# Performance work log

Hardware: AMD Instinct MI355X
Metric: run time of the kernel (lower is better)

The kernel has to match this reference:

```python
import jax, jax.numpy as jnp
import numpy as np

B, N, D, N_HOPS = 32, 1024, 128, 3
EPS = 1e-6


def setup_inputs() -> dict:
    key = jax.random.key(0)
    k1, k2, k3, k4 = jax.random.split(key, 4)
    # binary base adjacency (non-trainable buffer in the torch module)
    adj = (jax.random.uniform(k1, (N, N)) < 0.05).astype(jnp.float32)
    adj_weight = jax.random.uniform(k2, (B, N, N), dtype=jnp.float32)
    x = jax.random.normal(k3, (B, N, D), dtype=jnp.float32)
    W = jax.random.normal(k4, (D, D), dtype=jnp.float32) * 0.05
    b = jnp.zeros((D,), jnp.float32)
    a2 = jnp.ones((D,), jnp.float32)   # LayerNorm scale
    b2 = jnp.zeros((D,), jnp.float32)  # LayerNorm shift
    return {"x": x, "adj_weight": adj_weight, "adj": adj, "W": W, "b": b, "a2": a2, "b2": b2}


def _conv(x, adj_weight, adj):
    # adj_power squares the matrix each hop: hop h uses A^(2^h).
    # mask_h = (A^(2^h) == 1.0); weighted hop = (W^(2^h)) * mask_h.
    # propagate(edge_index from dense_to_sparse) == sum_j Wmask[b,j,i] * x[b,j]  (A^T x)
    A = adj            # [N, N]
    Wp = adj_weight    # [B, N, N]
    agg = jnp.zeros_like(x)
    for h in range(N_HOPS):
        mask = (A == 1.0).astype(x.dtype)          # [N, N]
        Wh = Wp * mask                              # [B, N, N]
        agg = agg + jnp.einsum('bji,bjd->bid', Wh, x)
        if h < N_HOPS - 1:
            A = A @ A
            Wp = jnp.matmul(Wp, Wp)
    return agg


def reference(x, adj_weight, adj, W, b, a2, b2):
    agg = _conv(x, adj_weight, adj)
    h = jnp.einsum('bnd,od->bno', agg, W) + b + x   # Linear + residual
    mean = jnp.mean(h, axis=-1, keepdims=True)
    std = jnp.std(h, axis=-1, keepdims=True, ddof=1)  # torch.std is unbiased
    y = a2 * (h - mean) / (std + EPS) + b2
    return y  # dropout p=0 (eval) -> identity
```

## Files before the change

kernel.cpp:

```cpp
#include <hip/hip_runtime.h>

#define NN 1024
#define BB 32
#define DD 128
#define EPSF 1e-6f
#define CAP 16384

typedef __bf16 bf16x8 __attribute__((ext_vector_type(8)));
typedef float  f32x4  __attribute__((ext_vector_type(4)));
typedef unsigned short u16x8 __attribute__((ext_vector_type(8)));

__device__ __forceinline__ float bf2f(unsigned short u) {
  union { unsigned int i; float f; } v; v.i = ((unsigned int)u) << 16; return v.f;
}
__device__ __forceinline__ unsigned short f2bf(float f) {
  union { float f; unsigned int i; } v; v.f = f;
  unsigned int r = v.i + 0x7fffu + ((v.i >> 16) & 1u);
  return (unsigned short)(r >> 16);
}


__global__ __launch_bounds__(256) void convert_wp(const float* __restrict__ src,
    unsigned short* __restrict__ Wp, unsigned short* __restrict__ WpT) {
  __shared__ float tile[64][65];
  const int b = blockIdx.z;
  const int c0 = blockIdx.x * 64, r0 = blockIdx.y * 64;
  const int t = threadIdx.x;
  const int rr = t >> 3, cb = (t & 7) * 8;
  const size_t base = (size_t)b * NN * NN;
#pragma unroll
  for (int p = 0; p < 2; ++p) {
    const int r = rr + p * 32;
    const float* srow = src + base + (size_t)(r0 + r) * NN + c0 + cb;
    f32x4 v0 = *(const f32x4*)srow;
    f32x4 v1 = *(const f32x4*)(srow + 4);
    u16x8 w;
#pragma unroll
    for (int j = 0; j < 4; ++j) { w[j] = f2bf(v0[j]); w[4 + j] = f2bf(v1[j]); }
    *(u16x8*)(Wp + base + (size_t)(r0 + r) * NN + c0 + cb) = w;
#pragma unroll
    for (int j = 0; j < 4; ++j) { tile[r][cb + j] = v0[j]; tile[r][cb + 4 + j] = v1[j]; }
  }
  __syncthreads();
#pragma unroll
  for (int p = 0; p < 2; ++p) {
    const int r = rr + p * 32;
    u16x8 w;
#pragma unroll
    for (int j = 0; j < 8; ++j) w[j] = f2bf(tile[cb + j][r]);
    *(u16x8*)(WpT + base + (size_t)(c0 + r) * NN + r0 + cb) = w;
  }
}

__global__ __launch_bounds__(256) void convert_x(const float* __restrict__ x,
    unsigned short* __restrict__ xT) {
  __shared__ float tile[32][33];
  const int b = blockIdx.z;
  const int d0 = blockIdx.x * 32, n0 = blockIdx.y * 32;
  const int tx = threadIdx.x, ty = threadIdx.y;
#pragma unroll
  for (int s = 0; s < 4; ++s) {
    int rr = ty + s * 8;
    tile[rr][tx] = x[(size_t)b * NN * DD + (size_t)(n0 + rr) * DD + d0 + tx];
  }
  __syncthreads();
#pragma unroll
  for (int s = 0; s < 4; ++s) {
    int rr = ty + s * 8;
    xT[(size_t)b * DD * NN + (size_t)(d0 + rr) * NN + n0 + tx] = f2bf(tile[tx][rr]);
  }
}

__global__ __launch_bounds__(256) void mask0cvt(const float* __restrict__ adj,
    unsigned char* __restrict__ mcode, unsigned short* __restrict__ adjbf,
    unsigned short* __restrict__ adjTbf) {
  __shared__ float tile[32][33];
  const int i0 = blockIdx.x * 32, j0 = blockIdx.y * 32;
  const int tx = threadIdx.x, ty = threadIdx.y;
#pragma unroll
  for (int s = 0; s < 4; ++s) {
    int rr = ty + s * 8;
    float v = adj[(size_t)(j0 + rr) * NN + i0 + tx];
    adjbf[(size_t)(j0 + rr) * NN + i0 + tx] = f2bf(v);
    tile[rr][tx] = v;
  }
  __syncthreads();
#pragma unroll
  for (int s = 0; s < 4; ++s) {
    int rr = ty + s * 8;
    float v = tile[tx][rr];
    adjTbf[(size_t)(i0 + rr) * NN + j0 + tx] = f2bf(v);
    mcode[(size_t)(i0 + rr) * NN + j0 + tx] = (v == 1.0f) ? 1 : 0;
  }
}

#define BM 128
#define BN 128
#define BK 32
#define NIT (NN / BK)

__device__ __forceinline__ void async_cp16(const void* g, void* l) {
  __builtin_amdgcn_global_load_lds((const __attribute__((address_space(1))) void*)g,
                                   (__attribute__((address_space(3))) void*)l, 16, 0, 0);
}

struct EpiWcomb {
  const unsigned short* WpT;
  const unsigned char* mcode;
  unsigned short* out;
  __device__ __forceinline__ void operator()(int b, int i, int j, float v) const {
    size_t bnn = (size_t)b * (size_t)NN * NN;
    size_t idx = (size_t)i * NN + j;
    unsigned char mc = mcode[idx];
    float r = (mc & 2) ? v : 0.f;
    if (mc & 1) r += bf2f(WpT[bnn + idx]);
    out[bnn + idx] = f2bf(r);
  }
};

struct EpiAgg {
  float* agg;
  __device__ __forceinline__ void operator()(int b, int i, int d, float v) const {
    agg[(size_t)b * NN * DD + (size_t)i * DD + d] = v;
  }
};

struct EpiSq1 {
  unsigned short* A2;
  unsigned short* A2T;
  unsigned char* mcode;
  __device__ __forceinline__ void operator()(int b, int m, int n, float v) const {
    unsigned short bv = f2bf(v);
    A2[(size_t)m * NN + n] = bv;
    A2T[(size_t)n * NN + m] = bv;
    if (v == 1.0f) mcode[(size_t)n * NN + m] |= 2;
  }
};

struct EpiSq2 {
  unsigned int* entries;
  int* nnz;
  __device__ __forceinline__ void operator()(int b, int m, int n, float v) const {
    if (v == 1.0f) {
      int idx = atomicAdd(nnz, 1);
      if (idx < CAP) entries[idx] = ((unsigned)m << 16) | (unsigned)n;
    }
  }
};

template <typename Epi>
__global__ __launch_bounds__(256) void gemm_bt(const unsigned short* __restrict__ Abase,
    const unsigned short* __restrict__ Bbase, size_t sA, size_t sB, int swz, Epi epi) {
  __shared__ __align__(16) unsigned short As[3 * BM * BK];
  __shared__ __align__(16) unsigned short Bs[3 * BN * BK];
  const int b = blockIdx.z;
  int bx = blockIdx.x, by = blockIdx.y;
  if (swz) {
    int lin = bx + (by << 3);
    int r = lin & 7, s = lin >> 3;
    bx = ((r & 3) << 1) | (s & 1);
    by = ((r >> 2) << 2) | (s >> 1);
  }
  const int tm = bx * BM;
  const int tn = by * BN;
  const unsigned short* A = Abase + (size_t)b * sA;
  const unsigned short* B = Bbase + (size_t)b * sB;
  const int tid = threadIdx.x;
  const int w = tid >> 6, l = tid & 63;
  const int lr = l >> 2, lc = l & 3;
  const int fr = l & 15, quad = l >> 4;
  const int moff = (w & 1) * 64, noff = (w >> 1) * 64;
  f32x4 acc[4][4];
#pragma unroll
  for (int mi = 0; mi < 4; ++mi)
#pragma unroll
    for (int ni = 0; ni < 4; ++ni) acc[mi][ni] = (f32x4){0.f, 0.f, 0.f, 0.f};

  auto issue = [&](int kt, int buf) {
    unsigned short* Ad = As + buf * (BM * BK);
    unsigned short* Bd = Bs + buf * (BN * BK);
#pragma unroll
    for (int s = 0; s < 2; ++s) {
      const int rb = (w + s * 4) * 16;
      int r = rb + lr;
      int kc = lc ^ ((r >> 1) & 3);
      async_cp16(A + (size_t)(tm + r) * NN + kt * BK + kc * 8, (void*)(Ad + rb * BK));
      async_cp16(B + (size_t)(tn + r) * NN + kt * BK + kc * 8, (void*)(Bd + rb * BK));
    }
  };
  auto compute = [&](int buf) {
    const unsigned short* Ab = As + buf * (BM * BK);
    const unsigned short* Bb = Bs + buf * (BN * BK);
    bf16x8 af[4], bfr[4];
#pragma unroll
    for (int mi = 0; mi < 4; ++mi) {
      int r = moff + mi * 16 + fr;
      int kc = quad ^ ((r >> 1) & 3);
      af[mi] = *(const bf16x8*)(Ab + r * BK + kc * 8);
    }
#pragma unroll
    for (int ni = 0; ni < 4; ++ni) {
      int r = noff + ni * 16 + fr;
      int kc = quad ^ ((r >> 1) & 3);
      bfr[ni] = *(const bf16x8*)(Bb + r * BK + kc * 8);
    }
#pragma unroll
    for (int mi = 0; mi < 4; ++mi)
#pragma unroll
      for (int ni = 0; ni < 4; ++ni)
        acc[mi][ni] = __builtin_amdgcn_mfma_f32_16x16x32_bf16(af[mi], bfr[ni], acc[mi][ni], 0, 0, 0);
  };

  issue(0, 0); issue(1, 1); issue(2, 2);
#pragma unroll 1
  for (int kt = 0; kt < NIT - 3; ++kt) {
    asm volatile("s_waitcnt vmcnt(8)" ::: "memory");
    __builtin_amdgcn_s_barrier();
    asm volatile("" ::: "memory");
    compute(kt % 3);
    asm volatile("" ::: "memory");
    __builtin_amdgcn_s_barrier();
    asm volatile("" ::: "memory");
    issue(kt + 3, kt % 3);
  }
  asm volatile("s_waitcnt vmcnt(8)" ::: "memory");
  __builtin_amdgcn_s_barrier();
  asm volatile("" ::: "memory");
  compute((NIT - 3) % 3);
  asm volatile("s_waitcnt vmcnt(4)" ::: "memory");
  __builtin_amdgcn_s_barrier();
  asm volatile("" ::: "memory");
  compute((NIT - 2) % 3);
  asm volatile("s_waitcnt vmcnt(0)" ::: "memory");
  __builtin_amdgcn_s_barrier();
  asm volatile("" ::: "memory");
  compute((NIT - 1) % 3);
  asm volatile("" ::: "memory");

#pragma unroll
  for (int mi = 0; mi < 4; ++mi)
#pragma unroll
    for (int ni = 0; ni < 4; ++ni)
#pragma unroll
      for (int t = 0; t < 4; ++t)
        epi(b, tm + moff + mi * 16 + quad * 4 + t, tn + noff + ni * 16 + fr, acc[mi][ni][t]);
}

__global__ __launch_bounds__(256) void hop2_fix(const unsigned short* __restrict__ Wp,
    const unsigned short* __restrict__ WpT, const int* __restrict__ nnz,
    const unsigned int* __restrict__ entries, unsigned short* __restrict__ WcombT) {
  int n = *nnz;
  if (n > CAP) n = CAP;
  if (n == 0) return;
  __shared__ float rbuf[256];
  const int b = blockIdx.x;
  const size_t bnn = (size_t)b * NN * NN;
  for (int e = blockIdx.y; e < n; e += gridDim.y) {
    unsigned int ent = entries[e];
    int j = ent >> 16, i = ent & 0xFFFF;
    float s = 0.f;
    for (int k = threadIdx.x; k < NN; k += 256) {
      float u = 0.f, v = 0.f;
      const unsigned short* wj  = Wp  + bnn + (size_t)j * NN;
      const unsigned short* wtk = WpT + bnn + (size_t)k * NN;
      const unsigned short* wk  = Wp  + bnn + (size_t)k * NN;
      const unsigned short* wti = WpT + bnn + (size_t)i * NN;
      for (int t = 0; t < NN; ++t) {
        u += bf2f(wj[t]) * bf2f(wtk[t]);
        v += bf2f(wk[t]) * bf2f(wti[t]);
      }
      s += u * v;
    }
    rbuf[threadIdx.x] = s;
    __syncthreads();
    for (int off = 128; off > 0; off >>= 1) {
      if (threadIdx.x < off) rbuf[threadIdx.x] += rbuf[threadIdx.x + off];
      __syncthreads();
    }
    if (threadIdx.x == 0) {
      size_t idx = bnn + (size_t)i * NN + j;
      WcombT[idx] = f2bf(bf2f(WcombT[idx]) + rbuf[0]);
    }
    __syncthreads();
  }
}

#define ROWS_PER_BLK 32
__global__ __launch_bounds__(256) void fused_out(const float* agg, const float* __restrict__ x,
    const float* __restrict__ W, const float* __restrict__ bias,
    const float* __restrict__ g2, const float* __restrict__ bsh, float* out) {
  __shared__ unsigned short Wl[128 * 136];
  __shared__ float ar[256];
  __shared__ float xr[256];
  __shared__ float wred[8];
  const int tid = threadIdx.x;
  for (int e = tid; e < 16384; e += 256) Wl[(e >> 7) * 136 + (e & 127)] = f2bf(W[e]);
  const int half = tid >> 7, o = tid & 127;
  const int w = tid >> 6, lane = tid & 63;
  const float bo = bias[o], go = g2[o], b2o = bsh[o];
  const size_t row0 = (size_t)blockIdx.x * ROWS_PER_BLK;
  for (int rr = 0; rr < ROWS_PER_BLK; rr += 2) {
    const size_t rbase = (row0 + rr) * DD;
    __syncthreads();
    ar[tid] = agg[rbase + tid];
    xr[tid] = x[rbase + tid];
    __syncthreads();
    float hv = bo + xr[half * 128 + o];
    const unsigned short* wrow = &Wl[o * 136];
    const float* arow = &ar[half * 128];
#pragma unroll
    for (int d8 = 0; d8 < 16; ++d8) {
      bf16x8 wv = *(const bf16x8*)(wrow + d8 * 8);
#pragma unroll
      for (int t = 0; t < 8; ++t) hv += (float)wv[t] * arow[d8 * 8 + t];
    }
    float s = hv, q = hv * hv;
#pragma unroll
    for (int off = 32; off > 0; off >>= 1) {
      s += __shfl_xor(s, off);
      q += __shfl_xor(q, off);
    }
    if (lane == 0) { wred[w] = s; wred[4 + w] = q; }
    __syncthreads();
    float st = wred[half * 2] + wred[half * 2 + 1];
    float qt = wred[4 + half * 2] + wred[4 + half * 2 + 1];
    float mean = st * (1.0f / 128.0f);
    float var = (qt - 128.0f * mean * mean) * (1.0f / 127.0f);
    var = fmaxf(var, 0.0f);
    float stdv = sqrtf(var);
    out[rbase + tid] = go * (hv - mean) / (stdv + EPSF) + b2o;
  }
}

extern "C" void kernel_launch(void* const* d_in, const int* in_sizes, int n_in,
                              void* d_out, int out_size, void* d_ws, size_t ws_size,
                              hipStream_t stream) {
  (void)in_sizes; (void)n_in; (void)out_size; (void)ws_size;
  const float* x    = (const float*)d_in[0];
  const float* adjw = (const float*)d_in[1];
  const float* adj  = (const float*)d_in[2];
  const float* W    = (const float*)d_in[3];
  const float* bias = (const float*)d_in[4];
  const float* a2   = (const float*)d_in[5];
  const float* b2   = (const float*)d_in[6];
  float* out = (float*)d_out;

  char* ws = (char*)d_ws;
  unsigned short* Wp_bf   = (unsigned short*)(ws);
  unsigned short* WpT_bf  = (unsigned short*)(ws + 67108864);
  unsigned short* WcombT  = (unsigned short*)(ws + 134217728);
  unsigned short* xT_bf   = (unsigned short*)(ws + 201326592);
  unsigned short* adj_bf  = (unsigned short*)(ws + 209715200);
  unsigned short* adjT_bf = (unsigned short*)(ws + 211812352);
  unsigned short* A2_bf   = (unsigned short*)(ws + 213909504);
  unsigned short* A2T_bf  = (unsigned short*)(ws + 216006656);
  unsigned char* mcode    = (unsigned char*)(ws + 218103808);
  unsigned int* entries   = (unsigned int*)(ws + 219152384);
  int* nnz2               = (int*)(ws + 219217920);
  float* agg = out;

  hipMemsetAsync(nnz2, 0, 4, stream);

  dim3 blk32(32, 8, 1);
  convert_wp<<<dim3(16, 16, 32), 256, 0, stream>>>(adjw, Wp_bf, WpT_bf);
  convert_x<<<dim3(4, 32, 32), blk32, 0, stream>>>(x, xT_bf);
  mask0cvt<<<dim3(32, 32, 1), blk32, 0, stream>>>(adj, mcode, adj_bf, adjT_bf);

  EpiSq1 es1{A2_bf, A2T_bf, mcode};
  gemm_bt<EpiSq1><<<dim3(8, 8, 1), 256, 0, stream>>>(adj_bf, adjT_bf, 0, 0, 1, es1);
  EpiSq2 es2{entries, nnz2};
  gemm_bt<EpiSq2><<<dim3(8, 8, 1), 256, 0, stream>>>(A2_bf, A2T_bf, 0, 0, 1, es2);

  EpiWcomb e1{WpT_bf, mcode, WcombT};
  gemm_bt<EpiWcomb><<<dim3(8, 8, 32), 256, 0, stream>>>(WpT_bf, Wp_bf,
      (size_t)NN * NN, (size_t)NN * NN, 1, e1);

  hop2_fix<<<dim3(32, 8, 1), 256, 0, stream>>>(Wp_bf, WpT_bf, nnz2, entries, WcombT);

  EpiAgg e2{agg};
  gemm_bt<EpiAgg><<<dim3(8, 1, 32), 256, 0, stream>>>(WcombT, xT_bf,
      (size_t)NN * NN, (size_t)DD * NN, 0, e2);

  fused_out<<<dim3(1024, 1, 1), 256, 0, stream>>>(agg, x, W, bias, a2, b2, out);
}
```

Measured before the change: 538.2 us.

## Rework GEMM pipeline with register staging, split-K atomics and fused mask-add loader

Replaces the async global-to-LDS triple-buffered GEMM with a register-staged double-buffered pipeline that raises occupancy through launch bounds. The small adjacency-squaring GEMMs and the aggregation GEMM now use split-K with fp32 atomic accumulation, which fills more CUs. Threshold scanning moves into separate scan kernels. The hop-0 masked WpT add moves from the Wcomb epilogue into the aggregation GEMM's A-operand loader. This adds memsets and atomic traffic, and it changes the rounding order, because the combined operand is rounded to bf16 after adding.

```diff
diff --git a/kernel.cpp b/kernel.cpp
--- a/kernel.cpp
+++ b/kernel.cpp
@@ -5,6 +5,7 @@
 #define DD 128
 #define EPSF 1e-6f
 #define CAP 16384
+#define NNNN ((size_t)NN * NN)
 
 typedef __bf16 bf16x8 __attribute__((ext_vector_type(8)));
 typedef float  f32x4  __attribute__((ext_vector_type(4)));
@@ -27,7 +28,7 @@
   const int c0 = blockIdx.x * 64, r0 = blockIdx.y * 64;
   const int t = threadIdx.x;
   const int rr = t >> 3, cb = (t & 7) * 8;
-  const size_t base = (size_t)b * NN * NN;
+  const size_t base = (size_t)b * NNNN;
 #pragma unroll
   for (int p = 0; p < 2; ++p) {
     const int r = rr + p * 32;
@@ -94,66 +95,107 @@
   }
 }
 
+__global__ __launch_bounds__(256) void scan_a2(const float* __restrict__ A2f,
+    unsigned short* __restrict__ A2, unsigned short* __restrict__ A2T,
+    unsigned char* __restrict__ mcode) {
+  __shared__ float tile[32][33];
+  const int m0 = blockIdx.x * 32, n0 = blockIdx.y * 32;
+  const int tx = threadIdx.x, ty = threadIdx.y;
+#pragma unroll
+  for (int s = 0; s < 4; ++s) {
+    int rr = ty + s * 8;
+    float v = A2f[(size_t)(m0 + rr) * NN + n0 + tx];
+    A2[(size_t)(m0 + rr) * NN + n0 + tx] = f2bf(v);
+    tile[rr][tx] = v;
+  }
+  __syncthreads();
+#pragma unroll
+  for (int s = 0; s < 4; ++s) {
+    int rr = ty + s * 8;
+    float v = tile[tx][rr];
+    A2T[(size_t)(n0 + rr) * NN + m0 + tx] = f2bf(v);
+    if (v == 1.0f) mcode[(size_t)(n0 + rr) * NN + m0 + tx] |= 2;
+  }
+}
+
+__global__ __launch_bounds__(256) void scan_a4(const float* __restrict__ A4f,
+    unsigned int* __restrict__ entries, int* __restrict__ nnz) {
+  int e = blockIdx.x * 256 + threadIdx.x;
+  float v = A4f[e];
+  if (v == 1.0f) {
+    int idx = atomicAdd(nnz, 1);
+    if (idx < CAP) entries[idx] = ((unsigned)(e >> 10) << 16) | (unsigned)(e & 1023);
+  }
+}
+
 #define BM 128
 #define BN 128
 #define BK 32
-#define NIT (NN / BK)
-
-__device__ __forceinline__ void async_cp16(const void* g, void* l) {
-  __builtin_amdgcn_global_load_lds((const __attribute__((address_space(1))) void*)g,
-                                   (__attribute__((address_space(3))) void*)l, 16, 0, 0);
-}
+
+struct LoadPlain {
+  const unsigned short* P;
+  size_t stride;
+  __device__ __forceinline__ u16x8 ld(int b, size_t off) const {
+    return *(const u16x8*)(P + (size_t)b * stride + off);
+  }
+};
+
+struct LoadComb {
+  const unsigned short* Wc;
+  const unsigned short* Wt;
+  const unsigned char* mc;
+  __device__ __forceinline__ u16x8 ld(int b, size_t off) const {
+    size_t o = (size_t)b * NNNN + off;
+    u16x8 a = *(const u16x8*)(Wc + o);
+    u16x8 w = *(const u16x8*)(Wt + o);
+    unsigned long long m = *(const unsigned long long*)(mc + off);
+    u16x8 r;
+#pragma unroll
+    for (int j = 0; j < 8; ++j) {
+      float s = bf2f(a[j]);
+      if ((m >> (8 * j)) & 1ull) s += bf2f(w[j]);
+      r[j] = f2bf(s);
+    }
+    return r;
+  }
+};
 
 struct EpiWcomb {
-  const unsigned short* WpT;
-  const unsigned char* mcode;
+  const unsigned char* mc;
   unsigned short* out;
   __device__ __forceinline__ void operator()(int b, int i, int j, float v) const {
-    size_t bnn = (size_t)b * (size_t)NN * NN;
     size_t idx = (size_t)i * NN + j;
-    unsigned char mc = mcode[idx];
-    float r = (mc & 2) ? v : 0.f;
-    if (mc & 1) r += bf2f(WpT[bnn + idx]);
-    out[bnn + idx] = f2bf(r);
+    out[(size_t)b * NNNN + idx] = (mc[idx] & 2) ? f2bf(v) : (unsigned short)0;
   }
 };
 
-struct EpiAgg {
+struct EpiAggAtom {
   float* agg;
   __device__ __forceinline__ void operator()(int b, int i, int d, float v) const {
-    agg[(size_t)b * NN * DD + (size_t)i * DD + d] = v;
+    atomicAdd(agg + (size_t)b * NN * DD + (size_t)i * DD + d, v);
   }
 };
 
-struct EpiSq1 {
-  unsigned short* A2;
-  unsigned short* A2T;
-  unsigned char* mcode;
+struct EpiSqAtom {
+  float* buf;
   __device__ __forceinline__ void operator()(int b, int m, int n, float v) const {
-    unsigned short bv = f2bf(v);
-    A2[(size_t)m * NN + n] = bv;
-    A2T[(size_t)n * NN + m] = bv;
-    if (v == 1.0f) mcode[(size_t)n * NN + m] |= 2;
+    atomicAdd(buf + (size_t)m * NN + n, v);
   }
 };
 
-struct EpiSq2 {
-  unsigned int* entries;
-  int* nnz;
-  __device__ __forceinline__ void operator()(int b, int m, int n, float v) const {
-    if (v == 1.0f) {
-      int idx = atomicAdd(nnz, 1);
-      if (idx < CAP) entries[idx] = ((unsigned)m << 16) | (unsigned)n;
-    }
-  }
-};
-
-template <typename Epi>
-__global__ __launch_bounds__(256) void gemm_bt(const unsigned short* __restrict__ Abase,
-    const unsigned short* __restrict__ Bbase, size_t sA, size_t sB, int swz, Epi epi) {
-  __shared__ __align__(16) unsigned short As[3 * BM * BK];
-  __shared__ __align__(16) unsigned short Bs[3 * BN * BK];
-  const int b = blockIdx.z;
+#define LGKM_BARRIER() do { \
+  asm volatile("s_waitcnt lgkmcnt(0)" ::: "memory"); \
+  __builtin_amdgcn_s_barrier(); \
+  asm volatile("" ::: "memory"); } while (0)
+
+template <typename LA, typename Epi>
+__global__ __launch_bounds__(256, 3) void gemm_pipe(LA la, LoadPlain lb,
+    int swz, int ksN, int nit, Epi epi) {
+  __shared__ __align__(16) unsigned short As[2 * BM * BK];
+  __shared__ __align__(16) unsigned short Bs[2 * BN * BK];
+  const int z = blockIdx.z;
+  const int b = z / ksN, ks = z - b * ksN;
+  const int kbase = ks * nit * BK;
   int bx = blockIdx.x, by = blockIdx.y;
   if (swz) {
     int lin = bx + (by << 3);
@@ -161,36 +203,42 @@
     bx = ((r & 3) << 1) | (s & 1);
     by = ((r >> 2) << 2) | (s >> 1);
   }
-  const int tm = bx * BM;
-  const int tn = by * BN;
-  const unsigned short* A = Abase + (size_t)b * sA;
-  const unsigned short* B = Bbase + (size_t)b * sB;
+  const int tm = bx * BM, tn = by * BN;
   const int tid = threadIdx.x;
   const int w = tid >> 6, l = tid & 63;
   const int lr = l >> 2, lc = l & 3;
   const int fr = l & 15, quad = l >> 4;
   const int moff = (w & 1) * 64, noff = (w >> 1) * 64;
+
+  const int r0 = w * 16 + lr, r1 = (w + 4) * 16 + lr;
+  const int kc0 = lc ^ ((r0 >> 1) & 3), kc1 = lc ^ ((r1 >> 1) & 3);
+  const size_t aoff0 = (size_t)(tm + r0) * NN + kbase + kc0 * 8;
+  const size_t aoff1 = (size_t)(tm + r1) * NN + kbase + kc1 * 8;
+  const size_t boff0 = (size_t)(tn + r0) * NN + kbase + kc0 * 8;
+  const size_t boff1 = (size_t)(tn + r1) * NN + kbase + kc1 * 8;
+  const int lsA0 = r0 * BK + lc * 8, lsA1 = r1 * BK + lc * 8;
+
   f32x4 acc[4][4];
 #pragma unroll
   for (int mi = 0; mi < 4; ++mi)
 #pragma unroll
     for (int ni = 0; ni < 4; ++ni) acc[mi][ni] = (f32x4){0.f, 0.f, 0.f, 0.f};
 
-  auto issue = [&](int kt, int buf) {
-    unsigned short* Ad = As + buf * (BM * BK);
-    unsigned short* Bd = Bs + buf * (BN * BK);
-#pragma unroll
-    for (int s = 0; s < 2; ++s) {
-      const int rb = (w + s * 4) * 16;
-      int r = rb + lr;
-      int kc = lc ^ ((r >> 1) & 3);
-      async_cp16(A + (size_t)(tm + r) * NN + kt * BK + kc * 8, (void*)(Ad + rb * BK));
-      async_cp16(B + (size_t)(tn + r) * NN + kt * BK + kc * 8, (void*)(Bd + rb * BK));
-    }
+  u16x8 va0, va1, vb0, vb1;
+  auto load_tile = [&](int kt) {
+    size_t kk = (size_t)kt * BK;
+    va0 = la.ld(b, aoff0 + kk); va1 = la.ld(b, aoff1 + kk);
+    vb0 = lb.ld(b, boff0 + kk); vb1 = lb.ld(b, boff1 + kk);
   };
-  auto compute = [&](int buf) {
-    const unsigned short* Ab = As + buf * (BM * BK);
-    const unsigned short* Bb = Bs + buf * (BN * BK);
+  auto write_tile = [&](int par) {
+    unsigned short* Ad = As + par * (BM * BK);
+    unsigned short* Bd = Bs + par * (BN * BK);
+    *(u16x8*)(Ad + lsA0) = va0; *(u16x8*)(Ad + lsA1) = va1;
+    *(u16x8*)(Bd + lsA0) = vb0; *(u16x8*)(Bd + lsA1) = vb1;
+  };
+  auto compute = [&](int par) {
+    const unsigned short* Ab = As + par * (BM * BK);
+    const unsigned short* Bb = Bs + par * (BN * BK);
     bf16x8 af[4], bfr[4];
 #pragma unroll
     for (int mi = 0; mi < 4; ++mi) {
@@ -211,31 +259,21 @@
         acc[mi][ni] = __builtin_amdgcn_mfma_f32_16x16x32_bf16(af[mi], bfr[ni], acc[mi][ni], 0, 0, 0);
   };
 
-  issue(0, 0); issue(1, 1); issue(2, 2);
+  load_tile(0);
+  write_tile(0);
+  load_tile(1);
+  LGKM_BARRIER();
 #pragma unroll 1
-  for (int kt = 0; kt < NIT - 3; ++kt) {
-    asm volatile("s_waitcnt vmcnt(8)" ::: "memory");
-    __builtin_amdgcn_s_barrier();
-    asm volatile("" ::: "memory");
-    compute(kt % 3);
-    asm volatile("" ::: "memory");
-    __builtin_amdgcn_s_barrier();
-    asm volatile("" ::: "memory");
-    issue(kt + 3, kt % 3);
-  }
-  asm volatile("s_waitcnt vmcnt(8)" ::: "memory");
-  __builtin_amdgcn_s_barrier();
-  asm volatile("" ::: "memory");
-  compute((NIT - 3) % 3);
-  asm volatile("s_waitcnt vmcnt(4)" ::: "memory");
-  __builtin_amdgcn_s_barrier();
-  asm volatile("" ::: "memory");
-  compute((NIT - 2) % 3);
-  asm volatile("s_waitcnt vmcnt(0)" ::: "memory");
-  __builtin_amdgcn_s_barrier();
-  asm volatile("" ::: "memory");
-  compute((NIT - 1) % 3);
-  asm volatile("" ::: "memory");
+  for (int kt = 0; kt < nit - 2; ++kt) {
+    compute(kt & 1);
+    write_tile((kt + 1) & 1);
+    load_tile(kt + 2);
+    LGKM_BARRIER();
+  }
+  compute((nit - 2) & 1);
+  write_tile((nit - 1) & 1);
+  LGKM_BARRIER();
+  compute((nit - 1) & 1);
 
 #pragma unroll
   for (int mi = 0; mi < 4; ++mi)
@@ -254,7 +292,7 @@
   if (n == 0) return;
   __shared__ float rbuf[256];
   const int b = blockIdx.x;
-  const size_t bnn = (size_t)b * NN * NN;
+  const size_t bnn = (size_t)b * NNNN;
   for (int e = blockIdx.y; e < n; e += gridDim.y) {
     unsigned int ent = entries[e];
     int j = ent >> 16, i = ent & 0xFFFF;
@@ -354,32 +392,39 @@
   unsigned short* adjT_bf = (unsigned short*)(ws + 211812352);
   unsigned short* A2_bf   = (unsigned short*)(ws + 213909504);
   unsigned short* A2T_bf  = (unsigned short*)(ws + 216006656);
-  unsigned char* mcode    = (unsigned char*)(ws + 218103808);
-  unsigned int* entries   = (unsigned int*)(ws + 219152384);
-  int* nnz2               = (int*)(ws + 219217920);
+  float* A2f              = (float*)(ws + 218103808);
+  float* A4f              = (float*)(ws + 222298112);
+  unsigned char* mcode    = (unsigned char*)(ws + 226492416);
+  unsigned int* entries   = (unsigned int*)(ws + 227540992);
+  int* nnz2               = (int*)(ws + 227606528);
   float* agg = out;
 
   hipMemsetAsync(nnz2, 0, 4, stream);
+  hipMemsetAsync(A2f, 0, (size_t)4 * NNNN, stream);
+  hipMemsetAsync(A4f, 0, (size_t)4 * NNNN, stream);
+  hipMemsetAsync(agg, 0, (size_t)BB * NN * DD * 4, stream);
 
   dim3 blk32(32, 8, 1);
   convert_wp<<<dim3(16, 16, 32), 256, 0, stream>>>(adjw, Wp_bf, WpT_bf);
   convert_x<<<dim3(4, 32, 32), blk32, 0, stream>>>(x, xT_bf);
   mask0cvt<<<dim3(32, 32, 1), blk32, 0, stream>>>(adj, mcode, adj_bf, adjT_bf);
 
-  EpiSq1 es1{A2_bf, A2T_bf, mcode};
-  gemm_bt<EpiSq1><<<dim3(8, 8, 1), 256, 0, stream>>>(adj_bf, adjT_bf, 0, 0, 1, es1);
-  EpiSq2 es2{entries, nnz2};
-  gemm_bt<EpiSq2><<<dim3(8, 8, 1), 256, 0, stream>>>(A2_bf, A2T_bf, 0, 0, 1, es2);
-
-  EpiWcomb e1{WpT_bf, mcode, WcombT};
-  gemm_bt<EpiWcomb><<<dim3(8, 8, 32), 256, 0, stream>>>(WpT_bf, Wp_bf,
-      (size_t)NN * NN, (size_t)NN * NN, 1, e1);
+  gemm_pipe<<<dim3(8, 8, 4), 256, 0, stream>>>(
+      LoadPlain{adj_bf, 0}, LoadPlain{adjT_bf, 0}, 0, 4, NN / 4 / BK, EpiSqAtom{A2f});
+  scan_a2<<<dim3(32, 32, 1), blk32, 0, stream>>>(A2f, A2_bf, A2T_bf, mcode);
+  gemm_pipe<<<dim3(8, 8, 4), 256, 0, stream>>>(
+      LoadPlain{A2_bf, 0}, LoadPlain{A2T_bf, 0}, 0, 4, NN / 4 / BK, EpiSqAtom{A4f});
+  scan_a4<<<dim3(4096, 1, 1), 256, 0, stream>>>(A4f, entries, nnz2);
+
+  gemm_pipe<<<dim3(8, 8, 32), 256, 0, stream>>>(
+      LoadPlain{WpT_bf, NNNN}, LoadPlain{Wp_bf, NNNN}, 1, 1, NN / BK,
+      EpiWcomb{mcode, WcombT});
 
   hop2_fix<<<dim3(32, 8, 1), 256, 0, stream>>>(Wp_bf, WpT_bf, nnz2, entries, WcombT);
 
-  EpiAgg e2{agg};
-  gemm_bt<EpiAgg><<<dim3(8, 1, 32), 256, 0, stream>>>(WcombT, xT_bf,
-      (size_t)NN * NN, (size_t)DD * NN, 0, e2);
+  gemm_pipe<<<dim3(8, 1, 64), 256, 0, stream>>>(
+      LoadComb{WcombT, WpT_bf, mcode}, LoadPlain{xT_bf, (size_t)DD * NN}, 0, 2,
+      NN / 2 / BK, EpiAggAtom{agg});
 
   fused_out<<<dim3(1024, 1, 1), 256, 0, stream>>>(agg, x, W, bias, a2, b2, out);
 }
```

Result: faster. 520.8 us (-3.2%).
